# Optimization experiments

Measured on AMD Instinct MI355X. Metric: run time of the kernel, lower is better.

The kernel has to match this reference:

```python
import jax, jax.numpy as jnp
import numpy as np

T = 256   # time steps
F = 64    # features per step
H = 32    # LSTM hidden size
FORGET_BIAS = 1.0  # TF LSTMCell default


def setup_inputs() -> dict:
    key = jax.random.key(0)
    k1, k2, k3 = jax.random.split(key, 3)
    B = 16384
    x = jax.random.normal(k1, (B, T * F), dtype=jnp.float32)
    W_lstm = jax.random.normal(k2, (F + H, 4 * H), dtype=jnp.float32) * 0.1
    b_lstm = jnp.zeros((4 * H,), dtype=jnp.float32)
    W_dense = jax.random.normal(k3, (H, 1), dtype=jnp.float32) * 0.1
    b_dense = jnp.zeros((1,), dtype=jnp.float32)
    return {"x": x, "W_lstm": W_lstm, "b_lstm": b_lstm,
            "W_dense": W_dense, "b_dense": b_dense}


def reference(x, W_lstm, b_lstm, W_dense, b_dense):
    B = x.shape[0]
    # [B, T*F] -> [T, B, F] for scan over time
    xs = x.reshape(B, T, F).transpose(1, 0, 2)

    def step(carry, x_t):
        c, h = carry
        # TF LSTMCell: concat([inputs, h]) @ kernel + bias, gate order i, j, f, o
        gates = jnp.concatenate([x_t, h], axis=-1) @ W_lstm + b_lstm
        i, j, f, o = jnp.split(gates, 4, axis=-1)
        c_new = c * jax.nn.sigmoid(f + FORGET_BIAS) + jax.nn.sigmoid(i) * jnp.tanh(j)
        h_new = jnp.tanh(c_new) * jax.nn.sigmoid(o)
        return (c_new, h_new), None

    c0 = jnp.zeros((B, H), dtype=x.dtype)
    h0 = jnp.zeros((B, H), dtype=x.dtype)
    (c_T, h_T), _ = jax.lax.scan(step, (c0, h0), xs)

    # dense(1) + ELU on the final hidden state, then flatten like predict()
    out = jax.nn.elu(h_T @ W_dense + b_dense)
    return out.reshape(-1)
```

## Files before the change

kernel.cpp:

```cpp
#include <hip/hip_runtime.h>
#include <stdint.h>

#define T_STEPS 256
#define F_IN 64
#define L2E 1.44269504f

typedef __bf16 bf16x8 __attribute__((ext_vector_type(8)));
typedef float f32x4 __attribute__((ext_vector_type(4)));
typedef uint32_t u32;
typedef uint32_t u32x4 __attribute__((ext_vector_type(4)));

#define GLDS16(gp, lp)                                                         \
    __builtin_amdgcn_global_load_lds(                                          \
        (const __attribute__((address_space(1))) unsigned int*)(gp),           \
        (__attribute__((address_space(3))) unsigned int*)(lp), 16, 0, 0)

static __device__ __forceinline__ u32 pk2(float lo, float hi) {
    unsigned short a = __builtin_bit_cast(unsigned short, (__bf16)lo);
    unsigned short b = __builtin_bit_cast(unsigned short, (__bf16)hi);
    return (u32)a | ((u32)b << 16);
}

__global__ __launch_bounds__(256, 1)
void lstm_fused(const float* __restrict__ x,
                const float* __restrict__ Wl,
                const float* __restrict__ bl,
                const float* __restrict__ Wd,
                const float* __restrict__ bd,
                float* __restrict__ out)
{
    __shared__ __align__(16) float xg[4][2][16][256];

    const int lane = threadIdx.x & 63;
    const int wid  = threadIdx.x >> 6;
    const int cl   = lane & 15;
    const int g4   = lane >> 4;
    const int rowBase = blockIdx.x * 64 + wid * 16;

#define GSC(q) (((q) >> 1) == 1 ? -2.0f * L2E : -L2E)

    bf16x8 wfrag[3][8];
#pragma unroll
    for (int kc = 0; kc < 3; ++kc) {
#pragma unroll
        for (int q = 0; q < 8; ++q) {
            bf16x8 v;
#pragma unroll
            for (int j = 0; j < 8; ++j)
                v[j] = (__bf16)(GSC(q) * Wl[(kc * 32 + g4 * 8 + j) * 128 + q * 16 + cl]);
            wfrag[kc][q] = v;
        }
    }

    f32x4 biasf[8];
#pragma unroll
    for (int q = 0; q < 8; ++q) {
#pragma unroll
        for (int r = 0; r < 4; ++r) {
            const int gate = q * 16 + g4 * 4 + r;
            biasf[q][r] = GSC(q) * (bl[gate] + ((q >> 1) == 2 ? 1.0f : 0.0f));
        }
    }
    const float bd0 = bd[0];
    float wdl[4], wdh[4];
#pragma unroll
    for (int r = 0; r < 4; ++r) {
        wdl[r] = Wd[4 * g4 + r];
        wdh[r] = Wd[16 + 4 * g4 + r];
    }

    const char* xbase = (const char*)(x + (size_t)rowBase * (size_t)(T_STEPS * F_IN));
    int loff[8];
#pragma unroll
    for (int k = 0; k < 8; ++k) loff[k] = ((lane ^ k) << 4);

    asm volatile("s_waitcnt vmcnt(0)" ::: "memory");
    __builtin_amdgcn_sched_barrier(0);

#define STAGE_GROUP(G, SL) do {                                                \
    _Pragma("unroll")                                                          \
    for (int r = 0; r < 16; ++r) {                                             \
        const char* gp = xbase + (size_t)r * (size_t)(T_STEPS * F_IN * 4)      \
                       + (size_t)(G) * 1024 + loff[r & 7];                     \
        GLDS16(gp, &xg[wid][SL][r][0]);                                        \
    }                                                                          \
} while (0)

    STAGE_GROUP(0, 0);
    STAGE_GROUP(1, 1);

    const int srcA = cl + 32 * (g4 & 1);
    const int srcB = srcA + 16;
    const int sel  = g4 >> 1;
    const int kswz = cl & 7;

    f32x4 csl = {0.f, 0.f, 0.f, 0.f};
    f32x4 csh = {0.f, 0.f, 0.f, 0.f};
    f32x4 hlv, hhv;
    u32x4 ahw = {0u, 0u, 0u, 0u};
    f32x4 accx[8];

#define CELL(AI, AJ, AF, AO, CS, HV) do {                                      \
    _Pragma("unroll")                                                          \
    for (int r = 0; r < 4; ++r) {                                              \
        float I  = __builtin_amdgcn_exp2f((AI)[r]);                            \
        float J  = __builtin_amdgcn_exp2f((AJ)[r]);                            \
        float Fv = __builtin_amdgcn_exp2f((AF)[r]);                            \
        float O  = __builtin_amdgcn_exp2f((AO)[r]);                            \
        float t3 = (1.0f + I) * (1.0f + J);                                    \
        float uu = 1.0f + Fv;                                                  \
        float np = __builtin_fmaf(J, 2.0f * L2E, -2.0f * L2E);                 \
        float r1 = __builtin_amdgcn_rcpf(t3 * uu);                             \
        float nm = __builtin_fmaf((CS)[r], t3, np * uu);                       \
        float cp = nm * r1;                                                    \
        float C  = __builtin_amdgcn_exp2f(cp);                                 \
        float r2 = __builtin_amdgcn_rcpf((1.0f + C) * (1.0f + O));             \
        (HV)[r] = (1.0f - C) * r2;                                             \
        (CS)[r] = cp;                                                          \
    }                                                                          \
} while (0)

#define XGATES(TT) do {                                                        \
    const float* base = &xg[wid][((TT) >> 2) & 1][cl][0];                      \
    const int c00 = (((TT) & 3) * 16 + 2 * g4) ^ kswz;                         \
    f32x4 xr0 = *(const f32x4*)(base + (size_t)( c00          ) * 4);          \
    f32x4 xr1 = *(const f32x4*)(base + (size_t)( c00 ^ 1      ) * 4);          \
    f32x4 xr2 = *(const f32x4*)(base + (size_t)( c00 ^ 8      ) * 4);          \
    f32x4 xr3 = *(const f32x4*)(base + (size_t)((c00 ^ 8) ^ 1 ) * 4);          \
    bf16x8 ax0, ax1;                                                           \
    _Pragma("unroll")                                                          \
    for (int j = 0; j < 4; ++j) {                                              \
        ax0[j]     = (__bf16)xr0[j];                                           \
        ax0[4 + j] = (__bf16)xr1[j];                                           \
        ax1[j]     = (__bf16)xr2[j];                                           \
        ax1[4 + j] = (__bf16)xr3[j];                                           \
    }                                                                          \
    _Pragma("unroll")                                                          \
    for (int q = 0; q < 8; ++q) {                                              \
        f32x4 a = __builtin_amdgcn_mfma_f32_16x16x32_bf16(wfrag[0][q], ax0, biasf[q], 0, 0, 0); \
        accx[q] = __builtin_amdgcn_mfma_f32_16x16x32_bf16(wfrag[1][q], ax1, a, 0, 0, 0);        \
    }                                                                          \
} while (0)

#define CHAIN() do {                                                           \
    bf16x8 ah = __builtin_bit_cast(bf16x8, ahw);                               \
    f32x4 acc[8];                                                              \
    _Pragma("unroll")                                                          \
    for (int q = 0; q < 8; ++q)                                                \
        acc[q] = __builtin_amdgcn_mfma_f32_16x16x32_bf16(wfrag[2][q], ah, accx[q], 0, 0, 0); \
    CELL(acc[0], acc[2], acc[4], acc[6], csl, hlv);                            \
    CELL(acc[1], acc[3], acc[5], acc[7], csh, hhv);                            \
    u32 W0 = pk2(hlv[0], hlv[1]);                                              \
    u32 W1 = pk2(hlv[2], hlv[3]);                                              \
    u32 W2 = pk2(hhv[0], hhv[1]);                                              \
    u32 W3 = pk2(hhv[2], hhv[3]);                                              \
    int A0 = __shfl((int)W0, srcA, 64), A1 = __shfl((int)W1, srcA, 64);        \
    int A2 = __shfl((int)W2, srcA, 64), A3 = __shfl((int)W3, srcA, 64);        \
    int B0 = __shfl((int)W0, srcB, 64), B1 = __shfl((int)W1, srcB, 64);        \
    int B2 = __shfl((int)W2, srcB, 64), B3 = __shfl((int)W3, srcB, 64);        \
    ahw[0] = (u32)(sel ? A2 : A0);                                             \
    ahw[1] = (u32)(sel ? A3 : A1);                                             \
    ahw[2] = (u32)(sel ? B2 : B0);                                             \
    ahw[3] = (u32)(sel ? B3 : B1);                                             \
} while (0)

    asm volatile("s_waitcnt vmcnt(16)" ::: "memory");
    __builtin_amdgcn_sched_barrier(0);
    XGATES(0);

    for (int G = 0; G < 64; ++G) {
        const int t0 = 4 * G;
        CHAIN(); XGATES(t0 + 1);
        CHAIN(); XGATES(t0 + 2);
        CHAIN(); XGATES(t0 + 3);
        CHAIN();
        if (G < 62) {
            STAGE_GROUP(G + 2, G & 1);
            asm volatile("s_waitcnt vmcnt(16)" ::: "memory");
        } else {
            asm volatile("s_waitcnt vmcnt(0)" ::: "memory");
        }
        __builtin_amdgcn_sched_barrier(0);
        const int tn = (t0 + 4 < T_STEPS) ? t0 + 4 : T_STEPS - 1;
        XGATES(tn);
    }
#undef CHAIN
#undef XGATES
#undef CELL
#undef STAGE_GROUP

    asm volatile("s_waitcnt vmcnt(0)" ::: "memory");

    float v = 0.f;
#pragma unroll
    for (int r = 0; r < 4; ++r) {
        v = __builtin_fmaf(hlv[r], wdl[r], v);
        v = __builtin_fmaf(hhv[r], wdh[r], v);
    }
    v += __shfl_xor(v, 16, 64);
    v += __shfl_xor(v, 32, 64);
    if (lane < 16) {
        float z = v + bd0;
        out[rowBase + lane] = z > 0.f ? z : (__expf(z) - 1.0f);
    }
}

extern "C" void kernel_launch(void* const* d_in, const int* in_sizes, int n_in,
                              void* d_out, int out_size, void* d_ws, size_t ws_size,
                              hipStream_t stream) {
    const float* x  = (const float*)d_in[0];
    const float* Wl = (const float*)d_in[1];
    const float* bl = (const float*)d_in[2];
    const float* Wd = (const float*)d_in[3];
    const float* bd = (const float*)d_in[4];
    float* out = (float*)d_out;

    const int rows = out_size;
    const int grid = (rows + 63) / 64;
    hipLaunchKernelGGL(lstm_fused, dim3(grid), dim3(256), 0, stream,
                       x, Wl, bl, Wd, bd, out);
}
```

Before: 242.0 us.

## Replace LDS-staged x loads with direct register prefetch ring of eight steps

Removes the global_load_lds staging into shared memory and the swizzled LDS reads. Each lane now loads its own x fragments straight from global memory into an 8-deep register ring, issuing the load for step t+8 while step t is computed. This drops the LDS round trip and the explicit vmcnt waits, at the cost of many more VGPRs (128 floats of prefetch per lane). It also relies on the compiler to insert waits, and the per-lane 16-byte loads are less coalesced across rows.

```diff
diff --git a/kernel.cpp b/kernel.cpp
--- a/kernel.cpp
+++ b/kernel.cpp
@@ -9,11 +9,6 @@
 typedef float f32x4 __attribute__((ext_vector_type(4)));
 typedef uint32_t u32;
 typedef uint32_t u32x4 __attribute__((ext_vector_type(4)));
-
-#define GLDS16(gp, lp)                                                         \
-    __builtin_amdgcn_global_load_lds(                                          \
-        (const __attribute__((address_space(1))) unsigned int*)(gp),           \
-        (__attribute__((address_space(3))) unsigned int*)(lp), 16, 0, 0)
 
 static __device__ __forceinline__ u32 pk2(float lo, float hi) {
     unsigned short a = __builtin_bit_cast(unsigned short, (__bf16)lo);
@@ -29,8 +24,6 @@
                 const float* __restrict__ bd,
                 float* __restrict__ out)
 {
-    __shared__ __align__(16) float xg[4][2][16][256];
-
     const int lane = threadIdx.x & 63;
     const int wid  = threadIdx.x >> 6;
     const int cl   = lane & 15;
@@ -69,30 +62,22 @@
         wdh[r] = Wd[16 + 4 * g4 + r];
     }
 
-    const char* xbase = (const char*)(x + (size_t)rowBase * (size_t)(T_STEPS * F_IN));
-    int loff[8];
-#pragma unroll
-    for (int k = 0; k < 8; ++k) loff[k] = ((lane ^ k) << 4);
-
-    asm volatile("s_waitcnt vmcnt(0)" ::: "memory");
-    __builtin_amdgcn_sched_barrier(0);
-
-#define STAGE_GROUP(G, SL) do {                                                \
-    _Pragma("unroll")                                                          \
-    for (int r = 0; r < 16; ++r) {                                             \
-        const char* gp = xbase + (size_t)r * (size_t)(T_STEPS * F_IN * 4)      \
-                       + (size_t)(G) * 1024 + loff[r & 7];                     \
-        GLDS16(gp, &xg[wid][SL][r][0]);                                        \
-    }                                                                          \
-} while (0)
-
-    STAGE_GROUP(0, 0);
-    STAGE_GROUP(1, 1);
+    const float* xrow = x + (size_t)(rowBase + cl) * (size_t)(T_STEPS * F_IN)
+                          + (size_t)(g4 * 8);
+
+    f32x4 xa[8], xb[8], xc[8], xd[8];
+
+#define LOADS(S, TT) do {                                                      \
+    const float* p = xrow + (size_t)(TT) * F_IN;                               \
+    xa[S] = *(const f32x4*)(p);                                                \
+    xb[S] = *(const f32x4*)(p + 4);                                            \
+    xc[S] = *(const f32x4*)(p + 32);                                           \
+    xd[S] = *(const f32x4*)(p + 36);                                           \
+} while (0)
 
     const int srcA = cl + 32 * (g4 & 1);
     const int srcB = srcA + 16;
     const int sel  = g4 >> 1;
-    const int kswz = cl & 7;
 
     f32x4 csl = {0.f, 0.f, 0.f, 0.f};
     f32x4 csh = {0.f, 0.f, 0.f, 0.f};
@@ -120,20 +105,14 @@
     }                                                                          \
 } while (0)
 
-#define XGATES(TT) do {                                                        \
-    const float* base = &xg[wid][((TT) >> 2) & 1][cl][0];                      \
-    const int c00 = (((TT) & 3) * 16 + 2 * g4) ^ kswz;                         \
-    f32x4 xr0 = *(const f32x4*)(base + (size_t)( c00          ) * 4);          \
-    f32x4 xr1 = *(const f32x4*)(base + (size_t)( c00 ^ 1      ) * 4);          \
-    f32x4 xr2 = *(const f32x4*)(base + (size_t)( c00 ^ 8      ) * 4);          \
-    f32x4 xr3 = *(const f32x4*)(base + (size_t)((c00 ^ 8) ^ 1 ) * 4);          \
+#define XGATES(S) do {                                                         \
     bf16x8 ax0, ax1;                                                           \
     _Pragma("unroll")                                                          \
     for (int j = 0; j < 4; ++j) {                                              \
-        ax0[j]     = (__bf16)xr0[j];                                           \
-        ax0[4 + j] = (__bf16)xr1[j];                                           \
-        ax1[j]     = (__bf16)xr2[j];                                           \
-        ax1[4 + j] = (__bf16)xr3[j];                                           \
+        ax0[j]     = (__bf16)xa[S][j];                                         \
+        ax0[4 + j] = (__bf16)xb[S][j];                                         \
+        ax1[j]     = (__bf16)xc[S][j];                                         \
+        ax1[4 + j] = (__bf16)xd[S][j];                                         \
     }                                                                          \
     _Pragma("unroll")                                                          \
     for (int q = 0; q < 8; ++q) {                                              \
@@ -164,32 +143,33 @@
     ahw[3] = (u32)(sel ? B3 : B1);                                             \
 } while (0)
 
-    asm volatile("s_waitcnt vmcnt(16)" ::: "memory");
-    __builtin_amdgcn_sched_barrier(0);
+    LOADS(0, 0); LOADS(1, 1); LOADS(2, 2); LOADS(3, 3);
+    LOADS(4, 4); LOADS(5, 5); LOADS(6, 6); LOADS(7, 7);
     XGATES(0);
 
-    for (int G = 0; G < 64; ++G) {
-        const int t0 = 4 * G;
-        CHAIN(); XGATES(t0 + 1);
-        CHAIN(); XGATES(t0 + 2);
-        CHAIN(); XGATES(t0 + 3);
-        CHAIN();
-        if (G < 62) {
-            STAGE_GROUP(G + 2, G & 1);
-            asm volatile("s_waitcnt vmcnt(16)" ::: "memory");
-        } else {
-            asm volatile("s_waitcnt vmcnt(0)" ::: "memory");
-        }
-        __builtin_amdgcn_sched_barrier(0);
-        const int tn = (t0 + 4 < T_STEPS) ? t0 + 4 : T_STEPS - 1;
-        XGATES(tn);
-    }
+#pragma unroll 1
+    for (int t = 0; t < T_STEPS - 8; t += 8) {
+        CHAIN(); LOADS(0, t +  8); XGATES(1);
+        CHAIN(); LOADS(1, t +  9); XGATES(2);
+        CHAIN(); LOADS(2, t + 10); XGATES(3);
+        CHAIN(); LOADS(3, t + 11); XGATES(4);
+        CHAIN(); LOADS(4, t + 12); XGATES(5);
+        CHAIN(); LOADS(5, t + 13); XGATES(6);
+        CHAIN(); LOADS(6, t + 14); XGATES(7);
+        CHAIN(); LOADS(7, t + 15); XGATES(0);
+    }
+    CHAIN(); XGATES(1);
+    CHAIN(); XGATES(2);
+    CHAIN(); XGATES(3);
+    CHAIN(); XGATES(4);
+    CHAIN(); XGATES(5);
+    CHAIN(); XGATES(6);
+    CHAIN(); XGATES(7);
+    CHAIN();
 #undef CHAIN
 #undef XGATES
 #undef CELL
-#undef STAGE_GROUP
-
-    asm volatile("s_waitcnt vmcnt(0)" ::: "memory");
+#undef LOADS
 
     float v = 0.f;
 #pragma unroll
```

Result: slower. 283.8 us (+17.3%).
